# Performance work log

Hardware: AMD Instinct MI355X
Metric: run time of the kernel (lower is better)

Reference implementation:

```python
import jax, jax.numpy as jnp
import numpy as np

N = 50000      # nodes
E = 800000     # edges (avg degree 16)
IN = 128       # in_features
OUT = 64       # out_features
NEG_SLOPE = 0.2


def setup_inputs() -> dict:
    key = jax.random.key(0)
    ks = jax.random.split(key, 6)
    x = jax.random.normal(ks[0], (N, IN), dtype=jnp.float32)
    edge_src = jax.random.randint(ks[1], (E,), 0, N, dtype=jnp.int32)  # row i of adj
    edge_dst = jax.random.randint(ks[2], (E,), 0, N, dtype=jnp.int32)  # col j of adj
    stdv = 1.0 / np.sqrt(OUT)
    W = jax.random.uniform(ks[3], (IN, OUT), jnp.float32, -stdv, stdv)
    a = jax.random.uniform(ks[4], (2 * OUT, 1), jnp.float32, -stdv, stdv)
    bias = jax.random.uniform(ks[5], (OUT,), jnp.float32, -stdv, stdv)
    return {"x": x, "W": W, "a": a, "bias": bias,
            "edge_src": edge_src, "edge_dst": edge_dst}


def reference(x, W, a, bias, edge_src, edge_dst):
    # h = input @ weight + bias    [N, OUT]
    h = x @ W + bias
    # Per-node attention halves: Wh1[i] + Wh2[j] == (e = Wh1 + Wh2.T)[i, j]
    Wh1 = h @ a[:OUT, 0]   # [N]
    Wh2 = h @ a[OUT:, 0]   # [N]
    # Edge-centric scores only where adj is nonzero (mirrors e.sparse_mask(adj))
    e = jax.nn.leaky_relu(Wh1[edge_src] + Wh2[edge_dst], NEG_SLOPE)  # [E]
    # Sparse softmax over dim=1 -> segment softmax grouped by source row
    emax = jax.ops.segment_max(e, edge_src, num_segments=N)          # [N]
    ex = jnp.exp(e - emax[edge_src])                                 # [E]
    denom = jax.ops.segment_sum(ex, edge_src, num_segments=N)        # [N]
    alpha = ex / denom[edge_src]                                     # [E]
    # out[i] = sum_j alpha_ij * h[j]  (sparse attention @ h)
    out = jax.ops.segment_sum(alpha[:, None] * h[edge_dst], edge_src,
                              num_segments=N)                        # [N, OUT]
    return out
```

## Files before the change

### kernel.cpp

```cpp
#include <hip/hip_runtime.h>
#include <math.h>


namespace {
constexpr int NN   = 50000;
constexpr int EE   = 800000;
constexpr int INF_ = 128;
constexpr int OUTF = 64;
constexpr float NEG_SLOPE = 0.2f;
constexpr int MAXDEG = 64;
constexpr int SCATTER_BLOCKS = 2048;
constexpr int GEMM_BLOCKS    = (NN + 63) / 64;
constexpr int MIX            = GEMM_BLOCKS * 3;
constexpr int TOTAL_BLOCKS   = SCATTER_BLOCKS + GEMM_BLOCKS;
}

__global__ __launch_bounds__(256)
void gat_fused(const float* __restrict__ x, const float* __restrict__ W,
               const float* __restrict__ av, const float* __restrict__ bias,
               const int* __restrict__ esrc, const int* __restrict__ edst,
               float* __restrict__ h, float* __restrict__ wh1,
               float* __restrict__ wh2, int* __restrict__ cnt,
               int* __restrict__ adj)
{
    const int id = blockIdx.x;
    bool is_gemm = false;
    int  ridx;
    if (id < MIX) {
        const int qd = id / 3, rm = id - qd * 3;
        if (rm == 2) { is_gemm = true; ridx = qd; }
        else         { ridx = qd * 2 + rm; }
    } else {
        ridx = (MIX / 3) * 2 + (id - MIX);
    }

    if (!is_gemm) {
        const int bucket = ridx & 7;
        const int slot   = ridx >> 3;
        const int nslots = SCATTER_BLOCKS >> 3;
        for (int e = slot * 256 + threadIdx.x; e < EE; e += nslots * 256) {
            const int s = esrc[e];
            if ((s & 7) == bucket) {
                const int p = atomicAdd(&cnt[s], 1);
                if (p < MAXDEG) adj[(size_t)s * MAXDEG + p] = edst[e];
            }
        }
        return;
    }

    __shared__ float xT[32 * 64];
    __shared__ float Wc[32 * 64];
    const int tid   = threadIdx.x;
    const int lane  = tid & 63;
    const int w     = tid >> 6;
    const int node0 = ridx * 64;

    const int ng   = lane & 3;
    const int fg   = lane >> 2;
    const int nloc = w * 16 + ng * 4;
    const int f0   = fg * 4;

    const int srow = tid & 63;
    const int sq   = tid >> 6;
    const int grow = node0 + srow;

    float acc[4][4] = {};

    for (int kc = 0; kc < INF_; kc += 32) {
        __syncthreads();
        float4 v0 = make_float4(0.f,0.f,0.f,0.f), v1 = v0;
        if (grow < NN) {
            const float4* xr = (const float4*)(x + (size_t)grow * INF_ + kc + sq * 8);
            v0 = xr[0]; v1 = xr[1];
        }
        {
            float* dst = &xT[(sq * 8) * 64 + srow];
            dst[0*64] = v0.x; dst[1*64] = v0.y; dst[2*64] = v0.z; dst[3*64] = v0.w;
            dst[4*64] = v1.x; dst[5*64] = v1.y; dst[6*64] = v1.z; dst[7*64] = v1.w;
        }
        {
            const float4* wr = (const float4*)(W + (size_t)kc * OUTF);
            float4* wc = (float4*)Wc;
            wc[tid]       = wr[tid];
            wc[tid + 256] = wr[tid + 256];
        }
        __syncthreads();
#pragma unroll 8
        for (int kk = 0; kk < 32; ++kk) {
            const float4 xv = *(const float4*)&xT[kk * 64 + nloc];
            const float4 wv = *(const float4*)&Wc[kk * 64 + f0];
            const float xa[4] = {xv.x, xv.y, xv.z, xv.w};
            const float wa[4] = {wv.x, wv.y, wv.z, wv.w};
#pragma unroll
            for (int i = 0; i < 4; ++i)
#pragma unroll
                for (int j = 0; j < 4; ++j) acc[i][j] += xa[i] * wa[j];
        }
    }

    const float4 bb = ((const float4*)bias)[fg];
    const float4 a1 = ((const float4*)av)[fg];
    const float4 a2 = ((const float4*)(av + OUTF))[fg];
    const float bbv[4] = {bb.x, bb.y, bb.z, bb.w};
    const float a1v[4] = {a1.x, a1.y, a1.z, a1.w};
    const float a2v[4] = {a2.x, a2.y, a2.z, a2.w};

#pragma unroll
    for (int i = 0; i < 4; ++i) {
        const int node = node0 + nloc + i;
        float p1 = 0.f, p2 = 0.f;
#pragma unroll
        for (int j = 0; j < 4; ++j) {
            acc[i][j] += bbv[j];
            p1 += acc[i][j] * a1v[j];
            p2 += acc[i][j] * a2v[j];
        }
        p1 += __shfl_xor(p1, 4); p1 += __shfl_xor(p1, 8);
        p1 += __shfl_xor(p1, 16); p1 += __shfl_xor(p1, 32);
        p2 += __shfl_xor(p2, 4); p2 += __shfl_xor(p2, 8);
        p2 += __shfl_xor(p2, 16); p2 += __shfl_xor(p2, 32);
        if (node < NN) {
            *(float4*)&h[(size_t)node * OUTF + f0] =
                make_float4(acc[i][0], acc[i][1], acc[i][2], acc[i][3]);
            if (fg == 0) { wh1[node] = p1; wh2[node] = p2; }
        }
    }
}

__global__ __launch_bounds__(256)
void gat_aggregate(const int* __restrict__ cnt, const int* __restrict__ adj,
                   const float* __restrict__ wh1, const float* __restrict__ wh2,
                   const float* __restrict__ h, float* __restrict__ out)
{
    __shared__ float s_alpha[16 * 65];
    __shared__ int   s_dst[16 * 65];
    const int tid  = threadIdx.x;
    const int wv   = tid >> 6;
    const int lane = tid & 63;
    const int q    = lane >> 4;
    const int f    = lane & 15;
    const int li   = wv * 4 + q;
    const int node = blockIdx.x * 16 + li;

    int deg = cnt[node];
    deg = deg > MAXDEG ? MAXDEG : deg;
    const float w1 = wh1[node];

    float ex[4]; int dl[4];
    float m = -INFINITY;
    float el[4];
#pragma unroll
    for (int k = 0; k < 4; ++k) {
        const int slot = f + 16 * k;
        int d = adj[(size_t)node * MAXDEG + slot];
        d = (slot < deg) ? d : 0;
        dl[k] = d;
        float v = w1 + wh2[d];
        v = v > 0.f ? v : NEG_SLOPE * v;
        el[k] = (slot < deg) ? v : -INFINITY;
        m = fmaxf(m, el[k]);
    }
    m = fmaxf(m, __shfl_xor(m, 1)); m = fmaxf(m, __shfl_xor(m, 2));
    m = fmaxf(m, __shfl_xor(m, 4)); m = fmaxf(m, __shfl_xor(m, 8));
    float s = 0.f;
#pragma unroll
    for (int k = 0; k < 4; ++k) {
        ex[k] = (f + 16 * k < deg) ? __expf(el[k] - m) : 0.f;
        s += ex[k];
    }
    s += __shfl_xor(s, 1); s += __shfl_xor(s, 2);
    s += __shfl_xor(s, 4); s += __shfl_xor(s, 8);
    const float inv = (deg > 0) ? 1.f / s : 0.f;

#pragma unroll
    for (int k = 0; k < 4; ++k) {
        s_alpha[li * 65 + f + 16 * k] = ex[k] * inv;
        s_dst  [li * 65 + f + 16 * k] = dl[k];
    }
    __syncthreads();

    float4 acc = make_float4(0.f, 0.f, 0.f, 0.f);
    const int base = li * 65;
    for (int j0 = 0; j0 < deg; j0 += 4) {
        const int i1 = j0 + 1 > 63 ? 63 : j0 + 1;
        const int i2 = j0 + 2 > 63 ? 63 : j0 + 2;
        const int i3 = j0 + 3 > 63 ? 63 : j0 + 3;
        const float a0 = s_alpha[base + j0], a1 = s_alpha[base + i1];
        const float a2 = s_alpha[base + i2], a3 = s_alpha[base + i3];
        const int   d0 = s_dst[base + j0],   d1 = s_dst[base + i1];
        const int   d2 = s_dst[base + i2],   d3 = s_dst[base + i3];
        const float4 v0 = *(const float4*)&h[(size_t)d0 * OUTF + f * 4];
        const float4 v1 = *(const float4*)&h[(size_t)d1 * OUTF + f * 4];
        const float4 v2 = *(const float4*)&h[(size_t)d2 * OUTF + f * 4];
        const float4 v3 = *(const float4*)&h[(size_t)d3 * OUTF + f * 4];
        acc.x += a0*v0.x + a1*v1.x + a2*v2.x + a3*v3.x;
        acc.y += a0*v0.y + a1*v1.y + a2*v2.y + a3*v3.y;
        acc.z += a0*v0.z + a1*v1.z + a2*v2.z + a3*v3.z;
        acc.w += a0*v0.w + a1*v1.w + a2*v2.w + a3*v3.w;
    }
    *(float4*)&out[(size_t)node * OUTF + f * 4] = acc;
}

extern "C" void kernel_launch(void* const* d_in, const int* in_sizes, int n_in,
                              void* d_out, int out_size, void* d_ws, size_t ws_size,
                              hipStream_t stream)
{
    const float* x    = (const float*)d_in[0];
    const float* W    = (const float*)d_in[1];
    const float* av   = (const float*)d_in[2];
    const float* bias = (const float*)d_in[3];
    const int*   esrc = (const int*)d_in[4];
    const int*   edst = (const int*)d_in[5];
    float* out = (float*)d_out;

    float* h   = (float*)d_ws;
    float* wh1 = h + (size_t)NN * OUTF;
    float* wh2 = wh1 + NN;
    int*   cnt = (int*)(wh2 + NN);
    int*   adj = cnt + NN;

    hipMemsetAsync(cnt, 0, NN * sizeof(int), stream);
    gat_fused<<<TOTAL_BLOCKS, 256, 0, stream>>>(
        x, W, av, bias, esrc, edst, h, wh1, wh2, cnt, adj);
    gat_aggregate<<<NN / 16, 256, 0, stream>>>(cnt, adj, wh1, wh2, h, out);
}
```

Baseline: 151.8 us.

## Replace global-atomic adjacency scatter with two-pass bucketed build and larger GEMM tiles

The per-edge global atomic scatter into the adjacency table is replaced by two passes. First each block sorts its chunk of edges into 256-node buckets in shared memory and appends them to per-bucket global staging arrays. Then a build kernel assembles each 128-node slice's adjacency in shared memory and writes it out coalesced. The GEMM also moves to 256-node tiles with an 8x8 register block per thread. The aim is to cut global atomic contention and scattered writes, at the cost of an extra launch, extra staging traffic, higher register pressure in the GEMM, and possible dropped edges if a bucket exceeds its fixed capacity.

```diff
diff --git a/kernel.cpp b/kernel.cpp
--- a/kernel.cpp
+++ b/kernel.cpp
@@ -1,6 +1,9 @@
 #include <hip/hip_runtime.h>
 #include <math.h>
 
+
+typedef unsigned long long u64;
+typedef unsigned int u32;
 
 namespace {
 constexpr int NN   = 50000;
@@ -9,10 +12,14 @@
 constexpr int OUTF = 64;
 constexpr float NEG_SLOPE = 0.2f;
 constexpr int MAXDEG = 64;
-constexpr int SCATTER_BLOCKS = 2048;
-constexpr int GEMM_BLOCKS    = (NN + 63) / 64;
-constexpr int MIX            = GEMM_BLOCKS * 3;
-constexpr int TOTAL_BLOCKS   = SCATTER_BLOCKS + GEMM_BLOCKS;
+
+constexpr int NBUCK   = 196;
+constexpr int BCAP    = 4608;
+constexpr int S1_CHUNK  = 2048;
+constexpr int S1_BLOCKS = (EE + S1_CHUNK - 1) / S1_CHUNK;
+constexpr int GEMM_BLOCKS = (NN + 255) / 256;
+constexpr int K1_BLOCKS = S1_BLOCKS + GEMM_BLOCKS;
+constexpr int S2_BLOCKS = NBUCK * 2;
 }
 
 __global__ __launch_bounds__(256)
@@ -20,63 +27,107 @@
                const float* __restrict__ av, const float* __restrict__ bias,
                const int* __restrict__ esrc, const int* __restrict__ edst,
                float* __restrict__ h, float* __restrict__ wh1,
-               float* __restrict__ wh2, int* __restrict__ cnt,
-               int* __restrict__ adj)
+               float* __restrict__ wh2, int* __restrict__ bcnt_g,
+               u64* __restrict__ bdata)
 {
-    const int id = blockIdx.x;
-    bool is_gemm = false;
-    int  ridx;
-    if (id < MIX) {
-        const int qd = id / 3, rm = id - qd * 3;
-        if (rm == 2) { is_gemm = true; ridx = qd; }
-        else         { ridx = qd * 2 + rm; }
-    } else {
-        ridx = (MIX / 3) * 2 + (id - MIX);
-    }
+    __shared__ u64 smem[5120];
+    const int id  = blockIdx.x;
+    const int tid = threadIdx.x;
+    const bool is_gemm = (id % 3 == 0) && (id / 3 < GEMM_BLOCKS);
 
     if (!is_gemm) {
-        const int bucket = ridx & 7;
-        const int slot   = ridx >> 3;
-        const int nslots = SCATTER_BLOCKS >> 3;
-        for (int e = slot * 256 + threadIdx.x; e < EE; e += nslots * 256) {
-            const int s = esrc[e];
-            if ((s & 7) == bucket) {
-                const int p = atomicAdd(&cnt[s], 1);
-                if (p < MAXDEG) adj[(size_t)s * MAXDEG + p] = edst[e];
+        int ridx = id - id / 3 - ((id % 3) ? 1 : 0);
+        if (id % 3 == 0) ridx = GEMM_BLOCKS * 2 + (id / 3 - GEMM_BLOCKS);
+        if (id / 3 >= GEMM_BLOCKS && id % 3 == 0) ridx = id - GEMM_BLOCKS;
+        else if (id % 3 != 0) ridx = id - id / 3 - 1;
+        if (ridx >= S1_BLOCKS) return;
+
+        u64* s_pairs = smem;
+        int* s_bcnt  = (int*)((char*)smem + 16384);
+        int* s_scan  = s_bcnt + NBUCK;
+        int* s_goff  = s_scan + NBUCK;
+
+        for (int i = tid; i < NBUCK; i += 256) s_bcnt[i] = 0;
+        __syncthreads();
+
+        const int e0  = ridx * S1_CHUNK;
+        const int tot = (EE - e0) < S1_CHUNK ? (EE - e0) : S1_CHUNK;
+
+        int mb[8], mp[8]; u64 mv[8]; int nmine = 0;
+#pragma unroll
+        for (int k = 0; k < 8; ++k) {
+            const int e = e0 + tid + k * 256;
+            if (e < e0 + tot) {
+                const int s = esrc[e], d = edst[e];
+                const int b = s >> 8;
+                mb[nmine] = b;
+                mp[nmine] = atomicAdd(&s_bcnt[b], 1);
+                mv[nmine] = ((u64)(u32)d << 32) | (u32)s;
+                ++nmine;
             }
         }
+        __syncthreads();
+        if (tid < NBUCK) s_scan[tid] = s_bcnt[tid];
+        __syncthreads();
+        for (int off = 1; off < NBUCK; off <<= 1) {
+            int v = 0;
+            if (tid < NBUCK && tid >= off) v = s_scan[tid - off];
+            __syncthreads();
+            if (tid < NBUCK && tid >= off) s_scan[tid] += v;
+            __syncthreads();
+        }
+        if (tid < NBUCK) {
+            const int c = s_bcnt[tid];
+            s_goff[tid] = c > 0 ? atomicAdd(&bcnt_g[tid], c) : 0;
+        }
+        __syncthreads();
+        for (int k = 0; k < nmine; ++k) {
+            const int b = mb[k];
+            s_pairs[s_scan[b] - s_bcnt[b] + mp[k]] = mv[k];
+        }
+        __syncthreads();
+        for (int i = tid; i < tot; i += 256) {
+            const u64 p = s_pairs[i];
+            const int s = (int)(u32)(p & 0xffffffffull);
+            const int b = s >> 8;
+            const int g = s_goff[b] + (i - (s_scan[b] - s_bcnt[b]));
+            if (g < BCAP) bdata[(size_t)b * BCAP + g] = p;
+        }
         return;
     }
 
-    __shared__ float xT[32 * 64];
-    __shared__ float Wc[32 * 64];
-    const int tid   = threadIdx.x;
+    float* xT = (float*)smem;
+    float* Wc = (float*)((char*)smem + 32768);
+    const int ridx  = id / 3;
     const int lane  = tid & 63;
     const int w     = tid >> 6;
-    const int node0 = ridx * 64;
-
-    const int ng   = lane & 3;
-    const int fg   = lane >> 2;
-    const int nloc = w * 16 + ng * 4;
-    const int f0   = fg * 4;
-
-    const int srow = tid & 63;
-    const int sq   = tid >> 6;
-    const int grow = node0 + srow;
-
-    float acc[4][4] = {};
+    const int node0 = ridx * 256;
+    const int ng    = lane & 7;
+    const int fg    = lane >> 3;
+    const int nbase = w * 64 + ng * 8;
+    const int f0    = fg * 8;
+
+    float acc[8][8] = {};
 
     for (int kc = 0; kc < INF_; kc += 32) {
         __syncthreads();
-        float4 v0 = make_float4(0.f,0.f,0.f,0.f), v1 = v0;
-        if (grow < NN) {
-            const float4* xr = (const float4*)(x + (size_t)grow * INF_ + kc + sq * 8);
-            v0 = xr[0]; v1 = xr[1];
-        }
         {
-            float* dst = &xT[(sq * 8) * 64 + srow];
-            dst[0*64] = v0.x; dst[1*64] = v0.y; dst[2*64] = v0.z; dst[3*64] = v0.w;
-            dst[4*64] = v1.x; dst[5*64] = v1.y; dst[6*64] = v1.z; dst[7*64] = v1.w;
+            const int grow = node0 + tid;
+            float4 v[8];
+#pragma unroll
+            for (int j = 0; j < 8; ++j) v[j] = make_float4(0.f, 0.f, 0.f, 0.f);
+            if (grow < NN) {
+                const float4* xr = (const float4*)(x + (size_t)grow * INF_ + kc);
+#pragma unroll
+                for (int j = 0; j < 8; ++j) v[j] = xr[j];
+            }
+#pragma unroll
+            for (int j = 0; j < 8; ++j) {
+                xT[(j*4+0)*256 + tid] = v[j].x;
+                xT[(j*4+1)*256 + tid] = v[j].y;
+                xT[(j*4+2)*256 + tid] = v[j].z;
+                xT[(j*4+3)*256 + tid] = v[j].w;
+            }
         }
         {
             const float4* wr = (const float4*)(W + (size_t)kc * OUTF);
@@ -85,45 +136,86 @@
             wc[tid + 256] = wr[tid + 256];
         }
         __syncthreads();
-#pragma unroll 8
+#pragma unroll 2
         for (int kk = 0; kk < 32; ++kk) {
-            const float4 xv = *(const float4*)&xT[kk * 64 + nloc];
-            const float4 wv = *(const float4*)&Wc[kk * 64 + f0];
-            const float xa[4] = {xv.x, xv.y, xv.z, xv.w};
-            const float wa[4] = {wv.x, wv.y, wv.z, wv.w};
-#pragma unroll
-            for (int i = 0; i < 4; ++i)
-#pragma unroll
-                for (int j = 0; j < 4; ++j) acc[i][j] += xa[i] * wa[j];
-        }
-    }
-
-    const float4 bb = ((const float4*)bias)[fg];
-    const float4 a1 = ((const float4*)av)[fg];
-    const float4 a2 = ((const float4*)(av + OUTF))[fg];
-    const float bbv[4] = {bb.x, bb.y, bb.z, bb.w};
-    const float a1v[4] = {a1.x, a1.y, a1.z, a1.w};
-    const float a2v[4] = {a2.x, a2.y, a2.z, a2.w};
-
-#pragma unroll
-    for (int i = 0; i < 4; ++i) {
-        const int node = node0 + nloc + i;
+            const float4 x0 = *(const float4*)&xT[kk * 256 + nbase];
+            const float4 x1 = *(const float4*)&xT[kk * 256 + nbase + 4];
+            const float4 w0 = *(const float4*)&Wc[kk * 64 + f0];
+            const float4 w1 = *(const float4*)&Wc[kk * 64 + f0 + 4];
+            const float xa[8] = {x0.x,x0.y,x0.z,x0.w,x1.x,x1.y,x1.z,x1.w};
+            const float wa[8] = {w0.x,w0.y,w0.z,w0.w,w1.x,w1.y,w1.z,w1.w};
+#pragma unroll
+            for (int i = 0; i < 8; ++i)
+#pragma unroll
+                for (int j = 0; j < 8; ++j) acc[i][j] += xa[i] * wa[j];
+        }
+    }
+
+    const float4 b0 = ((const float4*)bias)[fg*2];
+    const float4 b1 = ((const float4*)bias)[fg*2+1];
+    const float4 q0 = ((const float4*)av)[fg*2];
+    const float4 q1 = ((const float4*)av)[fg*2+1];
+    const float4 r0 = ((const float4*)(av + OUTF))[fg*2];
+    const float4 r1 = ((const float4*)(av + OUTF))[fg*2+1];
+    const float bb[8]  = {b0.x,b0.y,b0.z,b0.w,b1.x,b1.y,b1.z,b1.w};
+    const float a1v[8] = {q0.x,q0.y,q0.z,q0.w,q1.x,q1.y,q1.z,q1.w};
+    const float a2v[8] = {r0.x,r0.y,r0.z,r0.w,r1.x,r1.y,r1.z,r1.w};
+
+#pragma unroll
+    for (int i = 0; i < 8; ++i) {
+        const int node = node0 + nbase + i;
         float p1 = 0.f, p2 = 0.f;
 #pragma unroll
-        for (int j = 0; j < 4; ++j) {
-            acc[i][j] += bbv[j];
+        for (int j = 0; j < 8; ++j) {
+            acc[i][j] += bb[j];
             p1 += acc[i][j] * a1v[j];
             p2 += acc[i][j] * a2v[j];
         }
-        p1 += __shfl_xor(p1, 4); p1 += __shfl_xor(p1, 8);
-        p1 += __shfl_xor(p1, 16); p1 += __shfl_xor(p1, 32);
-        p2 += __shfl_xor(p2, 4); p2 += __shfl_xor(p2, 8);
-        p2 += __shfl_xor(p2, 16); p2 += __shfl_xor(p2, 32);
+        p1 += __shfl_xor(p1, 8); p1 += __shfl_xor(p1, 16); p1 += __shfl_xor(p1, 32);
+        p2 += __shfl_xor(p2, 8); p2 += __shfl_xor(p2, 16); p2 += __shfl_xor(p2, 32);
         if (node < NN) {
-            *(float4*)&h[(size_t)node * OUTF + f0] =
-                make_float4(acc[i][0], acc[i][1], acc[i][2], acc[i][3]);
+            float* hp = h + (size_t)node * OUTF + f0;
+            *(float4*)hp       = make_float4(acc[i][0], acc[i][1], acc[i][2], acc[i][3]);
+            *(float4*)(hp + 4) = make_float4(acc[i][4], acc[i][5], acc[i][6], acc[i][7]);
             if (fg == 0) { wh1[node] = p1; wh2[node] = p2; }
         }
+    }
+}
+
+__global__ __launch_bounds__(256)
+void gat_build(const int* __restrict__ bcnt_g, const u64* __restrict__ bdata,
+               int* __restrict__ cnt, int* __restrict__ adj)
+{
+    __shared__ int l_cnt[128];
+    __shared__ int l_adj[128 * 64];
+    const int tid    = threadIdx.x;
+    const int bid    = blockIdx.x;
+    const int bucket = bid >> 1;
+    const int node0  = bid << 7;
+    if (tid < 128) l_cnt[tid] = 0;
+    __syncthreads();
+
+    int n = bcnt_g[bucket];
+    n = n > BCAP ? BCAP : n;
+    for (int i = tid; i < n; i += 256) {
+        const u64 p = bdata[(size_t)bucket * BCAP + i];
+        const int s = (int)(u32)(p & 0xffffffffull);
+        const int d = (int)(u32)(p >> 32);
+        const int ln = s - node0;
+        if (ln >= 0 && ln < 128) {
+            const int pos = atomicAdd(&l_cnt[ln], 1);
+            if (pos < MAXDEG) l_adj[(ln << 6) + pos] = d;
+        }
+    }
+    __syncthreads();
+
+    const int nvalid = (NN - node0) < 128 ? (NN - node0) : 128;
+    if (nvalid <= 0) return;
+    for (int i = tid; i < nvalid * 64; i += 256)
+        adj[((size_t)node0 << 6) + i] = l_adj[i];
+    if (tid < nvalid) {
+        const int c = l_cnt[tid];
+        cnt[node0 + tid] = c > MAXDEG ? MAXDEG : c;
     }
 }
 
@@ -146,9 +238,8 @@
     deg = deg > MAXDEG ? MAXDEG : deg;
     const float w1 = wh1[node];
 
-    float ex[4]; int dl[4];
+    float ex[4]; int dl[4]; float el[4];
     float m = -INFINITY;
-    float el[4];
 #pragma unroll
     for (int k = 0; k < 4; ++k) {
         const int slot = f + 16 * k;
@@ -213,14 +304,17 @@
     const int*   edst = (const int*)d_in[5];
     float* out = (float*)d_out;
 
-    float* h   = (float*)d_ws;
-    float* wh1 = h + (size_t)NN * OUTF;
-    float* wh2 = wh1 + NN;
-    int*   cnt = (int*)(wh2 + NN);
-    int*   adj = cnt + NN;
-
-    hipMemsetAsync(cnt, 0, NN * sizeof(int), stream);
-    gat_fused<<<TOTAL_BLOCKS, 256, 0, stream>>>(
-        x, W, av, bias, esrc, edst, h, wh1, wh2, cnt, adj);
+    float* h      = (float*)d_ws;
+    float* wh1    = h + (size_t)NN * OUTF;
+    float* wh2    = wh1 + NN;
+    int*   cnt    = (int*)(wh2 + NN);
+    int*   adj    = cnt + NN;
+    int*   bcnt_g = adj + (size_t)NN * MAXDEG;
+    u64*   bdata  = (u64*)(bcnt_g + 200);
+
+    hipMemsetAsync(bcnt_g, 0, NBUCK * sizeof(int), stream);
+    gat_fused<<<K1_BLOCKS, 256, 0, stream>>>(
+        x, W, av, bias, esrc, edst, h, wh1, wh2, bcnt_g, bdata);
+    gat_build<<<S2_BLOCKS, 256, 0, stream>>>(bcnt_g, bdata, cnt, adj);
     gat_aggregate<<<NN / 16, 256, 0, stream>>>(cnt, adj, wh1, wh2, h, out);
 }
```

Result: faster. 143.7 us (-5.4%).
